# Kernel tuning notes

Measured on AMD Instinct MI355X. Metric: run time of the kernel, lower is better.

Reference implementation:

```python
import jax, jax.numpy as jnp
import numpy as np

N_NODES = 50000
N_EDGES = 800000
D = 64
P = 2.0  # init kwarg p


def setup_inputs() -> dict:
    key = jax.random.key(0)
    k1, k2, k3, k4 = jax.random.split(key, 4)
    X = jax.random.normal(k1, (N_NODES, D), dtype=jnp.float32)
    edge_index = jax.random.randint(k2, (2, N_EDGES), 0, N_NODES, dtype=jnp.int64)
    # SAGEConv params (Glorot-ish scale)
    s = 1.0 / np.sqrt(D)
    W_neigh = jax.random.normal(k3, (D, D), dtype=jnp.float32) * s
    W_self = jax.random.normal(k4, (D, D), dtype=jnp.float32) * s
    b = jnp.zeros((D,), dtype=jnp.float32)
    return {"X": X, "edge_index": edge_index, "W_neigh": W_neigh, "W_self": W_self, "b": b}


def _segment_mean(vals, idx, num_segments):
    # vals: [E, D], idx: [E] -> [num_segments, D]; mean with empty segments = 0
    s = jax.ops.segment_sum(vals, idx, num_segments=num_segments)
    cnt = jax.ops.segment_sum(jnp.ones((vals.shape[0],), vals.dtype), idx,
                              num_segments=num_segments)
    return s / jnp.maximum(cnt, 1.0)[:, None]


def reference(X, edge_index, W_neigh, W_self, b):
    src = edge_index[0]
    dst = edge_index[1]
    n = X.shape[0]
    # SAGEConv (mean aggregation): messages X[src] aggregated at dst
    agg = _segment_mean(X[src], dst, n)                      # [N, D]
    h = jax.nn.relu(agg @ W_neigh + X @ W_self + b)          # [N, D]
    # edge gather, |diff|^p, scatter-mean to src nodes, tanh
    m = jnp.abs(h[src] - h[dst]) ** P                        # [E, D]
    gg = jnp.tanh(_segment_mean(m, src, n))                  # [N, D]
    return gg
```

## Files before the change

kernel.cpp:

```cpp
#include <hip/hip_runtime.h>
#include <math.h>

#define D 64
#define SCAN_ELEMS 1024
#define STEP 256
#define SHIFT 8
#define PART_CHUNK 2048


typedef __attribute__((ext_vector_type(8))) short bf16x8;
typedef __attribute__((ext_vector_type(8))) unsigned short u16x8;
typedef __attribute__((ext_vector_type(4))) float f32x4;

__device__ inline unsigned short f2bf(float f) {
    unsigned u = __float_as_uint(f);
    return (unsigned short)((u + 0x7FFFu + ((u >> 16) & 1u)) >> 16);
}
__device__ inline float bf2f(unsigned short h) {
    return __uint_as_float(((unsigned)h) << 16);
}

__global__ __launch_bounds__(256) void part_hist_cvt(
    const int* __restrict__ src, const int* __restrict__ dst,
    int* __restrict__ cnt, int nE, int nN, int K, int WGs,
    const float* __restrict__ X, const float* __restrict__ Wn,
    const float* __restrict__ Ws, unsigned short* __restrict__ Xh,
    unsigned short* __restrict__ Whn, unsigned short* __restrict__ Whs,
    int n8x, int n8w) {
    __shared__ int lh[1024];
    int wg = blockIdx.x;
    if (wg >= WGs) {
        int i = (wg - WGs) * 256 + threadIdx.x;
        const float* in; unsigned short* outh; int idx;
        if (i < n8x) { in = X; outh = Xh; idx = i; }
        else if (i < n8x + n8w) { in = Wn; outh = Whn; idx = i - n8x; }
        else if (i < n8x + 2 * n8w) { in = Ws; outh = Whs; idx = i - n8x - n8w; }
        else return;
        const float4* p = (const float4*)in + (size_t)idx * 2;
        float4 a = p[0], b = p[1];
        union { unsigned short us[8]; uint4 v; } u;
        u.us[0] = f2bf(a.x); u.us[1] = f2bf(a.y); u.us[2] = f2bf(a.z); u.us[3] = f2bf(a.w);
        u.us[4] = f2bf(b.x); u.us[5] = f2bf(b.y); u.us[6] = f2bf(b.z); u.us[7] = f2bf(b.w);
        ((uint4*)outh)[idx] = u.v;
        return;
    }
    for (int i = threadIdx.x; i < K; i += 256) lh[i] = 0;
    __syncthreads();
    int base = wg * PART_CHUNK;
    int lim = min(base + PART_CHUNK, nE);
    for (int e = base + threadIdx.x; e < lim; e += 256) {
        int s = src[e], t = dst[e];
        atomicAdd(&lh[t >> SHIFT], 1);
        atomicAdd(&lh[(nN + s) >> SHIFT], 1);
    }
    __syncthreads();
    for (int b = threadIdx.x; b < K; b += 256) cnt[b * WGs + wg] = lh[b];
}

__global__ __launch_bounds__(256) void scan_part(
    const int* __restrict__ in, int* __restrict__ bsum, int n) {
    __shared__ int sdata[256];
    int b = blockIdx.x, t = threadIdx.x;
    int base = b * SCAN_ELEMS + t * 4;
    int s = 0;
#pragma unroll
    for (int k = 0; k < 4; ++k) { int i = base + k; if (i < n) s += in[i]; }
    sdata[t] = s;
    __syncthreads();
    for (int o = 128; o > 0; o >>= 1) {
        if (t < o) sdata[t] += sdata[t + o];
        __syncthreads();
    }
    if (t == 0) bsum[b] = sdata[0];
}

__global__ __launch_bounds__(256) void scan_tops(int* __restrict__ bsum, int nb) {
    __shared__ int sd[256];
    int t = threadIdx.x;
    int v = (t < nb) ? bsum[t] : 0;
    sd[t] = v;
    __syncthreads();
    for (int o = 1; o < 256; o <<= 1) {
        int u = (t >= o) ? sd[t - o] : 0;
        __syncthreads();
        sd[t] += u;
        __syncthreads();
    }
    if (t < nb) bsum[t] = sd[t] - v;
}

__global__ __launch_bounds__(256) void scan_final(
    const int* __restrict__ in, const int* __restrict__ bsum,
    int* __restrict__ out, int n) {
    __shared__ int sth[256];
    int b = blockIdx.x, t = threadIdx.x;
    int base = b * SCAN_ELEMS + t * 4;
    int v[4]; int s = 0;
#pragma unroll
    for (int k = 0; k < 4; ++k) { int i = base + k; v[k] = (i < n) ? in[i] : 0; s += v[k]; }
    sth[t] = s;
    __syncthreads();
    for (int o = 1; o < 256; o <<= 1) {
        int u = (t >= o) ? sth[t - o] : 0;
        __syncthreads();
        sth[t] += u;
        __syncthreads();
    }
    int run = sth[t] - s + bsum[b];
#pragma unroll
    for (int k = 0; k < 4; ++k) {
        int i = base + k;
        if (i < n) { out[i] = run; run += v[k]; }
    }
}

__global__ __launch_bounds__(256) void part_write(
    const int* __restrict__ src, const int* __restrict__ dst,
    const int* __restrict__ scanned, unsigned int* __restrict__ part,
    int nE, int nN, int K, int WGs) {
    __shared__ int cur[1024];
    int wg = blockIdx.x;
    for (int b = threadIdx.x; b < K; b += 256) cur[b] = scanned[b * WGs + wg];
    __syncthreads();
    int base = wg * PART_CHUNK;
    int lim = min(base + PART_CHUNK, nE);
    for (int e = base + threadIdx.x; e < lim; e += 256) {
        int s = src[e], t = dst[e];
        int k1 = t;
        int p1 = atomicAdd(&cur[k1 >> SHIFT], 1);
        part[p1] = ((unsigned)(k1 & (STEP - 1)) << 16) | (unsigned)s;
        int k2 = nN + s;
        int p2 = atomicAdd(&cur[k2 >> SHIFT], 1);
        part[p2] = ((unsigned)(k2 & (STEP - 1)) << 16) | (unsigned)t;
    }
}

__global__ __launch_bounds__(256) void csr_build(
    const unsigned int* __restrict__ part, const int* __restrict__ scanned,
    unsigned short* __restrict__ vals, int* __restrict__ off,
    int n2, int K, int WGs, int totalItems) {
    __shared__ int deg[STEP];
    __shared__ int pfx[STEP];
    int b = blockIdx.x, t = threadIdx.x;
    int base = scanned[b * WGs];
    int endi = (b + 1 < K) ? scanned[(b + 1) * WGs] : totalItems;

    deg[t] = 0;
    __syncthreads();
    for (int i = base + t; i < endi; i += 256)
        atomicAdd(&deg[part[i] >> 16], 1);
    __syncthreads();

    pfx[t] = deg[t];
    __syncthreads();
    for (int o = 1; o < STEP; o <<= 1) {
        int u = (t >= o) ? pfx[t - o] : 0;
        __syncthreads();
        pfx[t] += u;
        __syncthreads();
    }
    int ex = pfx[t] - deg[t];
    int g = b * STEP + t;
    if (g < n2) off[g] = base + ex;
    if (b == K - 1 && t == 0) off[n2] = totalItems;
    deg[t] = ex;
    __syncthreads();

    for (int i = base + t; i < endi; i += 256) {
        unsigned u = part[i];
        int l = (int)(u >> 16);
        int p = atomicAdd(&deg[l], 1);
        vals[base + p] = (unsigned short)(u & 0xffffu);
    }
}

#define ANODES 32
#define ROWB 144
__global__ __launch_bounds__(512) void agg_gemm(
    const unsigned short* __restrict__ Xh,
    const int* __restrict__ off,
    const unsigned short* __restrict__ vals,
    const unsigned short* __restrict__ Whn,
    const unsigned short* __restrict__ Whs,
    const float* __restrict__ bias,
    unsigned short* __restrict__ hh, int nNodes) {
    __shared__ __align__(16) unsigned short rows[2][32][72];

    int t = threadIdx.x;
    int w = t >> 6;
    int lane = t & 63;
    int st = (lane >> 4) & 3;
    int l15 = lane & 15;
    int grp = (lane >> 3) & 1;
    int q = lane & 7;
    int bb = blockIdx.x * ANODES;
    int node = bb + w * 4 + st;
    bool valid = node < nNodes;

    float acc[8];
#pragma unroll
    for (int j = 0; j < 8; ++j) acc[j] = 0.f;

    int beg = 0, deg = 0;
    if (valid) { beg = off[node]; deg = off[node + 1] - beg; }
    int chunks = (deg + 15) >> 4;
    int m1 = max(chunks, __shfl_xor(chunks, 16));
    int maxChunks = max(m1, __shfl_xor(m1, 32));

    for (int cc = 0; cc < maxChunks; ++cc) {
        int c = cc * 16;
        int idxv = 0;
        if (c + l15 < deg) idxv = vals[beg + c + l15];
        int cnt = deg - c;
#pragma unroll
        for (int u = 0; u < 8; ++u) {
            int e = grp * 8 + u;
            int idx = __shfl(idxv, st * 16 + e);
            u16x8 v = ((const u16x8*)(Xh + (size_t)idx * D))[q];
            float m = (e < cnt) ? 1.0f : 0.0f;
#pragma unroll
            for (int j = 0; j < 8; ++j) acc[j] += m * bf2f(v[j]);
        }
    }
#pragma unroll
    for (int j = 0; j < 8; ++j) acc[j] += __shfl_xor(acc[j], 8);

    if (grp == 0) {
        float inv = 1.0f / fmaxf((float)deg, 1.0f);
        u16x8 mv, xv;
        if (valid) {
#pragma unroll
            for (int j = 0; j < 8; ++j) mv[j] = f2bf(acc[j] * inv);
            xv = ((const u16x8*)(Xh + (size_t)node * D))[q];
        } else {
#pragma unroll
            for (int j = 0; j < 8; ++j) { mv[j] = 0; xv[j] = 0; }
        }
        int r = w * 4 + st;
        *(u16x8*)((char*)&rows[0][r][0] + q * 16) = mv;
        *(u16x8*)((char*)&rows[1][r][0] + q * 16) = xv;
    }
    __syncthreads();

    int rb = w >> 2;
    int ct = w & 3;
    int c = lane & 15;
    int hi = lane >> 4;
    f32x4 accm;
    float bv = bias[ct * 16 + c];
    accm[0] = bv; accm[1] = bv; accm[2] = bv; accm[3] = bv;
#pragma unroll
    for (int kh = 0; kh < 2; ++kh) {
        bf16x8 aA = *(const bf16x8*)((const char*)&rows[0][0][0] + (rb * 16 + c) * ROWB + kh * 64 + hi * 16);
        bf16x8 aX = *(const bf16x8*)((const char*)&rows[1][0][0] + (rb * 16 + c) * ROWB + kh * 64 + hi * 16);
        bf16x8 bN, bS;
        int kb = kh * 32 + hi * 8;
#pragma unroll
        for (int j = 0; j < 8; ++j) {
            bN[j] = (short)Whn[(size_t)(kb + j) * D + ct * 16 + c];
            bS[j] = (short)Whs[(size_t)(kb + j) * D + ct * 16 + c];
        }
        accm = __builtin_amdgcn_mfma_f32_16x16x32_bf16(aA, bN, accm, 0, 0, 0);
        accm = __builtin_amdgcn_mfma_f32_16x16x32_bf16(aX, bS, accm, 0, 0, 0);
    }
#pragma unroll
    for (int r = 0; r < 4; ++r) {
        int row = hi * 4 + r;
        int n2a = bb + rb * 16 + row;
        if (n2a < nNodes)
            hh[(size_t)n2a * D + ct * 16 + c] = f2bf(fmaxf(accm[r], 0.0f));
    }
}

__global__ __launch_bounds__(256) void m_gather(
    const unsigned short* __restrict__ hh,
    const int* __restrict__ off,
    const unsigned short* __restrict__ vals,
    float* __restrict__ out, int nNodes) {
    int t = threadIdx.x;
    int w = t >> 6;
    int lane = t & 63;
    int st = (lane >> 4) & 3;
    int l15 = lane & 15;
    int grp = (lane >> 3) & 1;
    int q = lane & 7;
    int node = blockIdx.x * 16 + w * 4 + st;
    bool valid = node < nNodes;

    u16x8 hv = {};
    int beg = 0, deg = 0;
    if (valid) {
        hv = ((const u16x8*)(hh + (size_t)node * D))[q];
        beg = off[nNodes + node];
        deg = off[nNodes + node + 1] - beg;
    }
    float hn[8];
#pragma unroll
    for (int j = 0; j < 8; ++j) hn[j] = bf2f(hv[j]);

    float acc[8];
#pragma unroll
    for (int j = 0; j < 8; ++j) acc[j] = 0.f;

    int chunks = (deg + 15) >> 4;
    int m1 = max(chunks, __shfl_xor(chunks, 16));
    int maxChunks = max(m1, __shfl_xor(m1, 32));

    for (int cc = 0; cc < maxChunks; ++cc) {
        int c = cc * 16;
        int idxv = 0;
        if (c + l15 < deg) idxv = vals[beg + c + l15];
        int cnt = deg - c;
#pragma unroll
        for (int u = 0; u < 8; ++u) {
            int e = grp * 8 + u;
            int idx = __shfl(idxv, st * 16 + e);
            u16x8 u0 = ((const u16x8*)(hh + (size_t)idx * D))[q];
            float m = (e < cnt) ? 1.0f : 0.0f;
#pragma unroll
            for (int j = 0; j < 8; ++j) {
                float d = hn[j] - bf2f(u0[j]);
                acc[j] += m * d * d;
            }
        }
    }
#pragma unroll
    for (int j = 0; j < 8; ++j) acc[j] += __shfl_xor(acc[j], 8);

    if (valid && grp == 0) {
        float inv = 1.0f / fmaxf((float)deg, 1.0f);
        float4 r0, r1;
        r0.x = tanhf(acc[0] * inv); r0.y = tanhf(acc[1] * inv);
        r0.z = tanhf(acc[2] * inv); r0.w = tanhf(acc[3] * inv);
        r1.x = tanhf(acc[4] * inv); r1.y = tanhf(acc[5] * inv);
        r1.z = tanhf(acc[6] * inv); r1.w = tanhf(acc[7] * inv);
        ((float4*)(out + (size_t)node * D))[q * 2] = r0;
        ((float4*)(out + (size_t)node * D))[q * 2 + 1] = r1;
    }
}

extern "C" void kernel_launch(void* const* d_in, const int* in_sizes, int n_in,
                              void* d_out, int out_size, void* d_ws, size_t ws_size,
                              hipStream_t stream) {
    const float* X  = (const float*)d_in[0];
    const int*   ei = (const int*)d_in[1];
    const float* Wn = (const float*)d_in[2];
    const float* Ws = (const float*)d_in[3];
    const float* b  = (const float*)d_in[4];
    float* out = (float*)d_out;

    int nNodes = in_sizes[0] / D;
    int nEdges = in_sizes[1] / 2;
    const int* src = ei;
    const int* dst = ei + nEdges;

    int n2 = 2 * nNodes;
    int K = (n2 + STEP - 1) / STEP;
    int WGs = (nEdges + PART_CHUNK - 1) / PART_CHUNK;
    int nCnt = K * WGs;
    int nb = (nCnt + SCAN_ELEMS - 1) / SCAN_ELEMS;
    int totalItems = 2 * nEdges;

    size_t o = 0;
    auto align4 = [](size_t x) { return (x + 3) & ~(size_t)3; };
    int* cnt     = (int*)d_ws;                 o = align4((size_t)nCnt);
    int* scanned = (int*)d_ws + o;             o = align4(o + (size_t)nCnt);
    int* bsum    = (int*)d_ws + o;             o = align4(o + 256);
    int* off     = (int*)d_ws + o;             o = align4(o + (size_t)n2 + 1);
    unsigned int* part = (unsigned int*)((int*)d_ws + o);
    o = align4(o + 2 * (size_t)nEdges);
    unsigned short* vals = (unsigned short*)((int*)d_ws + o);
    o = align4(o + (size_t)nEdges);
    unsigned short* Xh = (unsigned short*)((int*)d_ws + o);
    o = align4(o + (size_t)nNodes * D / 2);
    unsigned short* hh = (unsigned short*)((int*)d_ws + o);
    o = align4(o + (size_t)nNodes * D / 2);
    unsigned short* Whn = (unsigned short*)((int*)d_ws + o);
    o = align4(o + (size_t)(D * D) / 2);
    unsigned short* Whs = (unsigned short*)((int*)d_ws + o);

    int n8x = nNodes * D / 8;
    int n8w = D * D / 8;
    int cvtBlocks = (n8x + 2 * n8w + 255) / 256;

    part_hist_cvt<<<WGs + cvtBlocks, 256, 0, stream>>>(
        src, dst, cnt, nEdges, nNodes, K, WGs,
        X, Wn, Ws, Xh, Whn, Whs, n8x, n8w);
    scan_part<<<nb, 256, 0, stream>>>(cnt, bsum, nCnt);
    scan_tops<<<1, 256, 0, stream>>>(bsum, nb);
    scan_final<<<nb, 256, 0, stream>>>(cnt, bsum, scanned, nCnt);
    part_write<<<WGs, 256, 0, stream>>>(src, dst, scanned, part, nEdges, nNodes, K, WGs);
    csr_build<<<K, STEP, 0, stream>>>(part, scanned, vals, off, n2, K, WGs, totalItems);

    int aBlocks = (nNodes + ANODES - 1) / ANODES;
    agg_gemm<<<aBlocks, 512, 0, stream>>>(Xh, off, vals, Whn, Whs, b, hh, nNodes);
    int mBlocks = (nNodes + 15) / 16;
    m_gather<<<mBlocks, 256, 0, stream>>>(hh, off, vals, out, nNodes);
}
```

Measured before the change: 96.26 us.

## Sort nodes by degree to balance per-wave chunk loops in gather kernels

Builds a degree histogram inside csr_build, scans it, and counting-sorts node ids into a degree-ordered permutation for each direction. agg_gemm and m_gather then process nodes in that order, so the four nodes sharing a wave have similar degrees and the wave-wide max-chunk loop wastes fewer iterations. The cost is two extra small kernel launches, an indirection through perm, and scattered writes of hh rows.

```diff
diff --git a/kernel.cpp b/kernel.cpp
--- a/kernel.cpp
+++ b/kernel.cpp
@@ -74,9 +74,11 @@
     if (t == 0) bsum[b] = sdata[0];
 }
 
-__global__ __launch_bounds__(256) void scan_tops(int* __restrict__ bsum, int nb) {
+__global__ __launch_bounds__(256) void scan_tops(
+    int* __restrict__ bsum, int nb, int* __restrict__ cnt2) {
     __shared__ int sd[256];
     int t = threadIdx.x;
+    if (t < 128) cnt2[t] = 0;
     int v = (t < nb) ? bsum[t] : 0;
     sd[t] = v;
     __syncthreads();
@@ -138,20 +140,29 @@
 __global__ __launch_bounds__(256) void csr_build(
     const unsigned int* __restrict__ part, const int* __restrict__ scanned,
     unsigned short* __restrict__ vals, int* __restrict__ off,
-    int n2, int K, int WGs, int totalItems) {
+    int* __restrict__ cnt2, int n2, int nN, int K, int WGs, int totalItems) {
     __shared__ int deg[STEP];
     __shared__ int pfx[STEP];
+    __shared__ int h2[128];
     int b = blockIdx.x, t = threadIdx.x;
     int base = scanned[b * WGs];
     int endi = (b + 1 < K) ? scanned[(b + 1) * WGs] : totalItems;
 
     deg[t] = 0;
+    if (t < 128) h2[t] = 0;
     __syncthreads();
     for (int i = base + t; i < endi; i += 256)
         atomicAdd(&deg[part[i] >> 16], 1);
     __syncthreads();
 
-    pfx[t] = deg[t];
+    int g = b * STEP + t;
+    int dcount = deg[t];
+    if (g < n2) {
+        int sec = (g >= nN) ? 1 : 0;
+        atomicAdd(&h2[sec * 64 + min(dcount, 63)], 1);
+    }
+
+    pfx[t] = dcount;
     __syncthreads();
     for (int o = 1; o < STEP; o <<= 1) {
         int u = (t >= o) ? pfx[t - o] : 0;
@@ -159,8 +170,7 @@
         pfx[t] += u;
         __syncthreads();
     }
-    int ex = pfx[t] - deg[t];
-    int g = b * STEP + t;
+    int ex = pfx[t] - dcount;
     if (g < n2) off[g] = base + ex;
     if (b == K - 1 && t == 0) off[n2] = totalItems;
     deg[t] = ex;
@@ -171,6 +181,48 @@
         int l = (int)(u >> 16);
         int p = atomicAdd(&deg[l], 1);
         vals[base + p] = (unsigned short)(u & 0xffffu);
+    }
+    __syncthreads();
+    if (t < 128 && h2[t]) atomicAdd(&cnt2[t], h2[t]);
+}
+
+__global__ __launch_bounds__(128) void bin_scan(int* __restrict__ cnt2) {
+    __shared__ int sd[128];
+    int t = threadIdx.x;
+    int v = cnt2[t];
+    sd[t] = v;
+    __syncthreads();
+    for (int o = 1; o < 128; o <<= 1) {
+        int u = (t >= o) ? sd[t - o] : 0;
+        __syncthreads();
+        sd[t] += u;
+        __syncthreads();
+    }
+    cnt2[t] = sd[t] - v;
+}
+
+__global__ __launch_bounds__(256) void deg_scatter(
+    const int* __restrict__ off, int* __restrict__ cnt2,
+    unsigned short* __restrict__ perm, int n2, int nN) {
+    __shared__ int lh[128], lbase[128], lpos[128];
+    int t = threadIdx.x;
+    if (t < 128) { lh[t] = 0; lpos[t] = 0; }
+    __syncthreads();
+    int i = blockIdx.x * 256 + t;
+    int bin = -1, nodeid = 0;
+    if (i < n2) {
+        int d = off[i + 1] - off[i];
+        int sec = (i >= nN) ? 1 : 0;
+        bin = sec * 64 + min(d, 63);
+        nodeid = sec ? i - nN : i;
+        atomicAdd(&lh[bin], 1);
+    }
+    __syncthreads();
+    if (t < 128 && lh[t]) lbase[t] = atomicAdd(&cnt2[t], lh[t]);
+    __syncthreads();
+    if (bin >= 0) {
+        int p = lbase[bin] + atomicAdd(&lpos[bin], 1);
+        perm[p] = (unsigned short)nodeid;
     }
 }
 
@@ -180,6 +232,7 @@
     const unsigned short* __restrict__ Xh,
     const int* __restrict__ off,
     const unsigned short* __restrict__ vals,
+    const unsigned short* __restrict__ perm,
     const unsigned short* __restrict__ Whn,
     const unsigned short* __restrict__ Whs,
     const float* __restrict__ bias,
@@ -194,8 +247,9 @@
     int grp = (lane >> 3) & 1;
     int q = lane & 7;
     int bb = blockIdx.x * ANODES;
-    int node = bb + w * 4 + st;
-    bool valid = node < nNodes;
+    int rank = bb + w * 4 + st;
+    bool valid = rank < nNodes;
+    int node = valid ? (int)perm[rank] : 0;
 
     float acc[8];
 #pragma unroll
@@ -266,9 +320,11 @@
 #pragma unroll
     for (int r = 0; r < 4; ++r) {
         int row = hi * 4 + r;
-        int n2a = bb + rb * 16 + row;
-        if (n2a < nNodes)
-            hh[(size_t)n2a * D + ct * 16 + c] = f2bf(fmaxf(accm[r], 0.0f));
+        int rr = bb + rb * 16 + row;
+        if (rr < nNodes) {
+            int dstNode = perm[rr];
+            hh[(size_t)dstNode * D + ct * 16 + c] = f2bf(fmaxf(accm[r], 0.0f));
+        }
     }
 }
 
@@ -276,6 +332,7 @@
     const unsigned short* __restrict__ hh,
     const int* __restrict__ off,
     const unsigned short* __restrict__ vals,
+    const unsigned short* __restrict__ perm,
     float* __restrict__ out, int nNodes) {
     int t = threadIdx.x;
     int w = t >> 6;
@@ -284,8 +341,9 @@
     int l15 = lane & 15;
     int grp = (lane >> 3) & 1;
     int q = lane & 7;
-    int node = blockIdx.x * 16 + w * 4 + st;
-    bool valid = node < nNodes;
+    int rank = blockIdx.x * 16 + w * 4 + st;
+    bool valid = rank < nNodes;
+    int node = valid ? (int)perm[nNodes + rank] : 0;
 
     u16x8 hv = {};
     int beg = 0, deg = 0;
@@ -378,6 +436,9 @@
     unsigned short* Whn = (unsigned short*)((int*)d_ws + o);
     o = align4(o + (size_t)(D * D) / 2);
     unsigned short* Whs = (unsigned short*)((int*)d_ws + o);
+    o = align4(o + (size_t)(D * D) / 2);
+    int* cnt2 = (int*)d_ws + o;                o = align4(o + 128);
+    unsigned short* perm = (unsigned short*)((int*)d_ws + o);
 
     int n8x = nNodes * D / 8;
     int n8w = D * D / 8;
@@ -387,13 +448,17 @@
         src, dst, cnt, nEdges, nNodes, K, WGs,
         X, Wn, Ws, Xh, Whn, Whs, n8x, n8w);
     scan_part<<<nb, 256, 0, stream>>>(cnt, bsum, nCnt);
-    scan_tops<<<1, 256, 0, stream>>>(bsum, nb);
+    scan_tops<<<1, 256, 0, stream>>>(bsum, nb, cnt2);
     scan_final<<<nb, 256, 0, stream>>>(cnt, bsum, scanned, nCnt);
     part_write<<<WGs, 256, 0, stream>>>(src, dst, scanned, part, nEdges, nNodes, K, WGs);
-    csr_build<<<K, STEP, 0, stream>>>(part, scanned, vals, off, n2, K, WGs, totalItems);
+    csr_build<<<K, STEP, 0, stream>>>(part, scanned, vals, off, cnt2,
+                                      n2, nNodes, K, WGs, totalItems);
+    bin_scan<<<1, 128, 0, stream>>>(cnt2);
+    int sBlocks = (n2 + 255) / 256;
+    deg_scatter<<<sBlocks, 256, 0, stream>>>(off, cnt2, perm, n2, nNodes);
 
     int aBlocks = (nNodes + ANODES - 1) / ANODES;
-    agg_gemm<<<aBlocks, 512, 0, stream>>>(Xh, off, vals, Whn, Whs, b, hh, nNodes);
+    agg_gemm<<<aBlocks, 512, 0, stream>>>(Xh, off, vals, perm, Whn, Whs, b, hh, nNodes);
     int mBlocks = (nNodes + 15) / 16;
-    m_gather<<<mBlocks, 256, 0, stream>>>(hh, off, vals, out, nNodes);
-}
+    m_gather<<<mBlocks, 256, 0, stream>>>(hh, off, vals, perm, out, nNodes);
+}
```

Measured after the change: 105.3 us. 9.4% more time.
